# Performance work log

Hardware: AMD Instinct MI355X
Metric: run time of the kernel (lower is better)

The kernel has to match this reference:

```python
import jax, jax.numpy as jnp
import numpy as np

N_WIN = 8  # matches init kwarg n_win

def setup_inputs() -> dict:
    key = jax.random.key(0)
    k1, k2, k3 = jax.random.split(key, 3)
    c = 64
    x = jax.random.normal(k1, (1, c, 256, 256), dtype=jnp.float32)
    W = jax.random.normal(k2, (3 * c, c), dtype=jnp.float32) * 0.05
    bias = jax.random.normal(k3, (3 * c,), dtype=jnp.float32) * 0.05
    return {"x": x, "W": W, "bias": bias}

def reference(x, W, bias):
    b, c, h, w = x.shape
    n_h = n_w = N_WIN
    hs, ws = h // n_h, w // n_w
    nw = n_h * n_w
    # unfold into non-overlapping windows: [1, nw, hs*ws, c]
    xw = x.reshape(b, c, n_h, hs, n_w, ws)
    xw = xw.transpose(0, 2, 4, 3, 5, 1).reshape(1, nw, hs * ws, c)
    # shared QKV linear
    qkv = xw @ W.T + bias
    q, k, v = qkv[..., :c], qkv[..., c:2 * c], qkv[..., 2 * c:3 * c]
    # region-level routing via mean-pooled tokens
    q_r = q.mean(axis=2)  # [1, nw, c]
    k_r = k.mean(axis=2)
    a_r = jax.nn.relu(jnp.einsum('bic,bjc->bij', q_r, k_r))  # [1, nw, nw]
    # mix windows: a_r @ flattened(k/q) == window-mixing einsum
    k_m = jnp.einsum('bij,bjtc->bitc', a_r, k)
    q_m = jnp.einsum('bij,bjtc->bitc', a_r, q)
    # relu-gated windowed attention
    attn = jax.nn.relu(jnp.einsum('bitc,bisc->bits', q_m, k_m))  # [1, nw, T, T]
    o = jnp.einsum('bits,bisc->bitc', attn, v)  # [1, nw, T, c]
    # fold back to image
    o = o.reshape(b, n_h, n_w, hs, ws, c).transpose(0, 5, 1, 3, 2, 4).reshape(b, c, h, w)
    return o
```

## Files before the change

### kernel.cpp

```cpp
#include <hip/hip_runtime.h>

typedef _Float16 half_t;
typedef __attribute__((ext_vector_type(8))) _Float16 half8;
typedef __attribute__((ext_vector_type(4))) _Float16 half4;
typedef __attribute__((ext_vector_type(4))) float floatx4;
typedef __attribute__((ext_vector_type(16))) float floatx16;

#define MFMA16(A, B, C) __builtin_amdgcn_mfma_f32_16x16x32_f16((A), (B), (C), 0, 0, 0)
#define MFMA32(A, B, C) __builtin_amdgcn_mfma_f32_32x32x16_f16((A), (B), (C), 0, 0, 0)

__global__ __launch_bounds__(256) void k_qkv(
    const float* __restrict__ x, const float* __restrict__ W,
    const float* __restrict__ bias, half_t* __restrict__ q,
    half_t* __restrict__ k, half_t* __restrict__ vT,
    float* __restrict__ qsum, float* __restrict__ ksum) {
  __shared__ __align__(16) char smem[52736];
  half_t(*Xs)[72] = (half_t(*)[72])smem;
  half_t(*Ws)[72] = (half_t(*)[72])(smem + 18432);
  half_t(*S1)[136] = (half_t(*)[136])smem;
  half_t(*S2)[136] = (half_t(*)[136])(smem + 34816);
  float* qs_l = (float*)(smem + 52224);
  float* ks_l = qs_l + 64;
  const int w = blockIdx.y;
  const int tx = blockIdx.x;
  const int t0 = tx * 128;
  const int ih = w >> 3, iw = w & 7;
  const int xbase = ih * 8192 + iw * 32 + tx * 1024;
  const int tid = threadIdx.x;

  for (int i = tid; i < 2048; i += 256) {
    const int c = i >> 5, g = i & 31;
    const int tt = (g >> 3) * 32 + (g & 7) * 4;
    const floatx4 v =
        *(const floatx4*)&x[c * 65536 + xbase + (g >> 3) * 256 + (g & 7) * 4];
    #pragma unroll
    for (int p = 0; p < 4; p++) Xs[tt + p][c] = (half_t)v[p];
  }
  for (int i = tid; i < 3072; i += 256) {
    const int o = i >> 4, c4 = (i & 15) * 4;
    const floatx4 v = *(const floatx4*)&W[o * 64 + c4];
    half4 hv;
    #pragma unroll
    for (int p = 0; p < 4; p++) hv[p] = (half_t)v[p];
    *(half4*)&Ws[o][c4] = hv;
  }
  if (tid < 64) { qs_l[tid] = 0.f; ks_l[tid] = 0.f; }
  __syncthreads();

  const int wave = tid >> 6, lane = tid & 63;
  const int lrow = lane & 15, lq = lane >> 4;
  const int rbase = (wave >> 1) * 64;
  const int cbase = (wave & 1) * 96;

  floatx4 acc[4][6];
  const floatx4 z = {0.f, 0.f, 0.f, 0.f};
  #pragma unroll
  for (int mt = 0; mt < 4; mt++)
    #pragma unroll
    for (int nt = 0; nt < 6; nt++) acc[mt][nt] = z;

  #pragma unroll
  for (int kf = 0; kf < 2; kf++) {
    const int koff = kf * 32 + lq * 8;
    half8 a[4], b[6];
    #pragma unroll
    for (int mt = 0; mt < 4; mt++)
      a[mt] = *(const half8*)&Xs[rbase + mt * 16 + lrow][koff];
    #pragma unroll
    for (int nt = 0; nt < 6; nt++)
      b[nt] = *(const half8*)&Ws[cbase + nt * 16 + lrow][koff];
    #pragma unroll
    for (int mt = 0; mt < 4; mt++)
      #pragma unroll
      for (int nt = 0; nt < 6; nt++)
        acc[mt][nt] = MFMA16(a[mt], b[nt], acc[mt][nt]);
  }
  __syncthreads();

  #pragma unroll
  for (int nt = 0; nt < 6; nt++) {
    const int o = cbase + nt * 16 + lrow;
    const float bs = bias[o];
    if (o < 128) {
      float s = 0.f;
      #pragma unroll
      for (int mt = 0; mt < 4; mt++) {
        const int tr = rbase + mt * 16 + lq * 4;
        #pragma unroll
        for (int r = 0; r < 4; r++) {
          const float v = acc[mt][nt][r] + bs;
          S1[tr + r][o] = (half_t)v;
          s += v;
        }
      }
      if (o < 64) atomicAdd(&qs_l[o], s);
      else atomicAdd(&ks_l[o - 64], s);
    } else {
      const int oc = o - 128;
      #pragma unroll
      for (int mt = 0; mt < 4; mt++) {
        const int tr = rbase + mt * 16 + lq * 4;
        half4 pk;
        #pragma unroll
        for (int r = 0; r < 4; r++) pk[r] = (half_t)(acc[mt][nt][r] + bs);
        *(half4*)&S2[oc][tr] = pk;
      }
    }
  }
  __syncthreads();

  for (int idx = tid; idx < 3072; idx += 256) {
    if (idx < 2048) {
      const int t = idx >> 4, seg = idx & 15;
      const half8 v = *(const half8*)&S1[t][seg * 8];
      if (seg < 8)
        *(half8*)&q[w * 65536 + (t0 + t) * 64 + seg * 8] = v;
      else
        *(half8*)&k[w * 65536 + (t0 + t) * 64 + (seg - 8) * 8] = v;
    } else {
      const int i2 = idx - 2048;
      const int oc = i2 >> 4, seg = i2 & 15;
      *(half8*)&vT[w * 65536 + oc * 1024 + t0 + seg * 8] =
          *(const half8*)&S2[oc][seg * 8];
    }
  }
  if (tid < 64) {
    atomicAdd(&qsum[w * 64 + tid], qs_l[tid]);
    atomicAdd(&ksum[w * 64 + tid], ks_l[tid]);
  }
}

__global__ __launch_bounds__(256) void k_mix(const half_t* __restrict__ q,
                                             const half_t* __restrict__ k,
                                             const float* __restrict__ qsum,
                                             const float* __restrict__ ksum,
                                             half_t* __restrict__ qm,
                                             half_t* __restrict__ km) {
  __shared__ __align__(16) half_t qh[64][72];
  __shared__ __align__(16) half_t kh[64][72];
  __shared__ __align__(16) half_t arL[64][72];
  const half_t* __restrict__ src = blockIdx.y ? k : q;
  half_t* __restrict__ dst = blockIdx.y ? km : qm;
  const int tid = threadIdx.x;
  const int wave = tid >> 6, lane = tid & 63;
  const int ln31 = lane & 31;
  const int hk8 = (lane >> 5) * 8;
  const int lrow = lane & 15, lq = lane >> 4;

  const int pos0 = blockIdx.x * 256 + wave * 64 + ln31;
  half8 bB[2][4];
  #pragma unroll
  for (int t32 = 0; t32 < 2; t32++)
    #pragma unroll
    for (int kk = 0; kk < 4; kk++)
      #pragma unroll
      for (int jj = 0; jj < 8; jj++)
        bB[t32][kk][jj] =
            src[(kk * 16 + hk8 + jj) * 65536 + pos0 + t32 * 32];

  for (int e = tid; e < 1024; e += 256) {
    const int i = e >> 4, c4 = (e & 15) * 4;
    const floatx4 sq = *(const floatx4*)&qsum[i * 64 + c4];
    const floatx4 sk = *(const floatx4*)&ksum[i * 64 + c4];
    #pragma unroll
    for (int p = 0; p < 4; p++) {
      qh[i][c4 + p] = (half_t)sq[p];
      kh[i][c4 + p] = (half_t)sk[p];
    }
  }
  __syncthreads();

  {
    floatx4 ac[4];
    const floatx4 z = {0.f, 0.f, 0.f, 0.f};
    #pragma unroll
    for (int nt = 0; nt < 4; nt++) ac[nt] = z;
    #pragma unroll
    for (int kf = 0; kf < 2; kf++) {
      const int koff = kf * 32 + lq * 8;
      const half8 aF = *(const half8*)&qh[wave * 16 + lrow][koff];
      #pragma unroll
      for (int nt = 0; nt < 4; nt++) {
        const half8 bF = *(const half8*)&kh[nt * 16 + lrow][koff];
        ac[nt] = MFMA16(aF, bF, ac[nt]);
      }
    }
    const float scale = 1.f / (1024.f * 1024.f);
    #pragma unroll
    for (int nt = 0; nt < 4; nt++)
      #pragma unroll
      for (int r = 0; r < 4; r++) {
        const float v = ac[nt][r] * scale;
        arL[wave * 16 + lq * 4 + r][nt * 16 + lrow] =
            (half_t)(v > 0.f ? v : 0.f);
      }
  }
  __syncthreads();

  half8 aA[2][4];
  #pragma unroll
  for (int mt = 0; mt < 2; mt++)
    #pragma unroll
    for (int kk = 0; kk < 4; kk++)
      aA[mt][kk] = *(const half8*)&arL[mt * 32 + ln31][kk * 16 + hk8];

  #pragma unroll
  for (int t32 = 0; t32 < 2; t32++) {
    const int pos = pos0 + t32 * 32;
    floatx16 c0, c1;
    #pragma unroll
    for (int r = 0; r < 16; r++) { c0[r] = 0.f; c1[r] = 0.f; }
    #pragma unroll
    for (int kk = 0; kk < 4; kk++) {
      c0 = MFMA32(aA[0][kk], bB[t32][kk], c0);
      c1 = MFMA32(aA[1][kk], bB[t32][kk], c1);
    }
    const int h4 = (lane >> 5) * 4;
    #pragma unroll
    for (int r = 0; r < 16; r++) {
      const int row = (r & 3) + h4 + 8 * (r >> 2);
      dst[row * 65536 + pos] = (half_t)c0[r];
      dst[(32 + row) * 65536 + pos] = (half_t)c1[r];
    }
  }
}

__global__ __launch_bounds__(256, 2) void k_attn(const half_t* __restrict__ qm,
                                                 const half_t* __restrict__ km,
                                                 const half_t* __restrict__ vT,
                                                 float* __restrict__ out) {
  __shared__ __align__(16) char smem[55296];
  char* const VsB = smem;
  char* const StB = smem + 18432;
  const int w = blockIdx.x;
  const int t0 = blockIdx.y * 128;
  const int tid = threadIdx.x;
  const int wave = tid >> 6, lane = tid & 63;
  const int ln31 = lane & 31;
  const int hk8 = (lane >> 5) * 8, hk4 = (lane >> 5) * 4;
  const int w32 = wave * 32;
  const int wbase = w * 65536;

  auto vs_ptr = [&](int c, int sbyte) -> char* {
    return VsB + c * 288 + (sbyte ^ ((c & 15) << 4));
  };
  auto st_ptr = [&](int t, int sbyte) -> char* {
    return StB + t * 288 + (sbyte ^ ((t & 15) << 4));
  };

  half8 bQ[4][4];
  #pragma unroll
  for (int tt = 0; tt < 4; tt++)
    #pragma unroll
    for (int kk = 0; kk < 4; kk++)
      bQ[tt][kk] = *(const half8*)&qm[wbase + (t0 + tt * 32 + ln31) * 64 +
                                      kk * 16 + hk8];

  floatx16 oacc[2];
  #pragma unroll
  for (int ct = 0; ct < 2; ct++)
    #pragma unroll
    for (int r = 0; r < 16; r++) oacc[ct][r] = 0.f;

  half8 vpre[4], aK[4];
  #pragma unroll
  for (int j = 0; j < 4; j++) {
    const int idx = j * 256 + tid;
    const int c = idx >> 4, so = (idx & 15) * 8;
    vpre[j] = *(const half8*)&vT[wbase + c * 1024 + so];
  }
  #pragma unroll
  for (int kk = 0; kk < 4; kk++)
    aK[kk] = *(const half8*)&km[wbase + (w32 + ln31) * 64 + kk * 16 + hk8];

  for (int sc = 0; sc < 8; sc++) {
    floatx16 sacc[4];
    #pragma unroll
    for (int tt = 0; tt < 4; tt++)
      #pragma unroll
      for (int r = 0; r < 16; r++) sacc[tt][r] = 0.f;
    __builtin_amdgcn_s_setprio(1);
    #pragma unroll
    for (int kk = 0; kk < 4; kk++)
      #pragma unroll
      for (int tt = 0; tt < 4; tt++)
        sacc[tt] = MFMA32(aK[kk], bQ[tt][kk], sacc[tt]);
    __builtin_amdgcn_s_setprio(0);

    __syncthreads();

    #pragma unroll
    for (int j = 0; j < 4; j++) {
      const int idx = j * 256 + tid;
      const int c = idx >> 4;
      *(half8*)vs_ptr(c, (idx & 15) * 16) = vpre[j];
    }
    #pragma unroll
    for (int tt = 0; tt < 4; tt++) {
      const int t = tt * 32 + ln31;
      #pragma unroll
      for (int g = 0; g < 4; g++) {
        const int s = w32 + g * 8 + hk4;
        half4 pk;
        #pragma unroll
        for (int p = 0; p < 4; p++) {
          const float v = sacc[tt][g * 4 + p];
          pk[p] = (half_t)(v > 0.f ? v : 0.f);
        }
        *(half4*)st_ptr(t, s * 2) = pk;
      }
    }
    half8 aKn[4];
    if (sc < 7) {
      const int s0n = (sc + 1) * 128;
      #pragma unroll
      for (int j = 0; j < 4; j++) {
        const int idx = j * 256 + tid;
        const int c = idx >> 4, so = (idx & 15) * 8;
        vpre[j] = *(const half8*)&vT[wbase + c * 1024 + s0n + so];
      }
      #pragma unroll
      for (int kk = 0; kk < 4; kk++)
        aKn[kk] = *(const half8*)&km[wbase + (s0n + w32 + ln31) * 64 +
                                     kk * 16 + hk8];
    }
    __syncthreads();

    __builtin_amdgcn_s_setprio(1);
    #pragma unroll
    for (int kk = 0; kk < 8; kk++) {
      const half8 bS = *(const half8*)st_ptr(w32 + ln31, (kk * 16 + hk8) * 2);
      #pragma unroll
      for (int ct = 0; ct < 2; ct++) {
        const half8 aV =
            *(const half8*)vs_ptr(ct * 32 + ln31, (kk * 16 + hk8) * 2);
        oacc[ct] = MFMA32(aV, bS, oacc[ct]);
      }
    }
    __builtin_amdgcn_s_setprio(0);
    if (sc < 7) {
      #pragma unroll
      for (int kk = 0; kk < 4; kk++) aK[kk] = aKn[kk];
    }
  }

  const int ih = w >> 3, iw = w & 7;
  const int obase = ih * 8192 + iw * 32;
  const int tb = ((t0 + w32) >> 5) * 256 + ln31;
  const int h4 = (lane >> 5) * 4;
  #pragma unroll
  for (int ct = 0; ct < 2; ct++) {
    #pragma unroll
    for (int r = 0; r < 16; r++) {
      const int c = ct * 32 + (r & 3) + h4 + 8 * (r >> 2);
      out[c * 65536 + obase + tb] = oacc[ct][r];
    }
  }
}

extern "C" void kernel_launch(void* const* d_in, const int* in_sizes, int n_in,
                              void* d_out, int out_size, void* d_ws, size_t ws_size,
                              hipStream_t stream) {
  const float* x = (const float*)d_in[0];
  const float* W = (const float*)d_in[1];
  const float* bias = (const float*)d_in[2];
  float* out = (float*)d_out;

  half_t* q = (half_t*)d_ws;
  half_t* k = q + 4194304;
  half_t* vT = k + 4194304;
  half_t* qm = vT + 4194304;
  half_t* km = qm + 4194304;
  float* qsum = (float*)(km + 4194304);
  float* ksum = qsum + 4096;

  hipMemsetAsync(qsum, 0, 2 * 4096 * sizeof(float), stream);
  k_qkv<<<dim3(8, 64), 256, 0, stream>>>(x, W, bias, q, k, vT, qsum, ksum);
  k_mix<<<dim3(256, 2), 256, 0, stream>>>(q, k, qsum, ksum, qm, km);
  k_attn<<<dim3(64, 8), 256, 0, stream>>>(qm, km, vT, out);
}
```

Before: 116.4 us.

## Halve per-block tiles in qkv and mix kernels, use lgkm-only barrier in attn

The QKV projection kernel now processes 64 tokens per block instead of 128 and the window-mixing kernel 128 positions per block instead of 256, doubling their grid sizes to raise occupancy and parallelism across CUs. Shared memory in k_qkv shrinks accordingly. In the attention kernel, __syncthreads is replaced with a custom barrier that waits only on LDS counters (lgkmcnt) and not on outstanding global loads, so the V/K prefetches can stay in flight across the barrier. Smaller tiles add more redundant W loads and more atomics on the per-window sums.

```diff
diff --git a/kernel.cpp b/kernel.cpp
--- a/kernel.cpp
+++ b/kernel.cpp
@@ -9,30 +9,39 @@
 #define MFMA16(A, B, C) __builtin_amdgcn_mfma_f32_16x16x32_f16((A), (B), (C), 0, 0, 0)
 #define MFMA32(A, B, C) __builtin_amdgcn_mfma_f32_32x32x16_f16((A), (B), (C), 0, 0, 0)
 
+__device__ __forceinline__ void lds_barrier() {
+  __builtin_amdgcn_sched_barrier(0);
+  asm volatile("s_waitcnt lgkmcnt(0)\n\ts_barrier" ::: "memory");
+  __builtin_amdgcn_sched_barrier(0);
+}
+
 __global__ __launch_bounds__(256) void k_qkv(
     const float* __restrict__ x, const float* __restrict__ W,
     const float* __restrict__ bias, half_t* __restrict__ q,
     half_t* __restrict__ k, half_t* __restrict__ vT,
     float* __restrict__ qsum, float* __restrict__ ksum) {
-  __shared__ __align__(16) char smem[52736];
+  __shared__ __align__(16) char smem[37376];
   half_t(*Xs)[72] = (half_t(*)[72])smem;
-  half_t(*Ws)[72] = (half_t(*)[72])(smem + 18432);
+  half_t(*Ws)[72] = (half_t(*)[72])(smem + 9216);
   half_t(*S1)[136] = (half_t(*)[136])smem;
-  half_t(*S2)[136] = (half_t(*)[136])(smem + 34816);
-  float* qs_l = (float*)(smem + 52224);
+  half_t(*S2)[72] = (half_t(*)[72])(smem + 17408);
+  float* qs_l = (float*)(smem + 36864);
   float* ks_l = qs_l + 64;
   const int w = blockIdx.y;
   const int tx = blockIdx.x;
-  const int t0 = tx * 128;
+  const int t0 = tx * 64;
   const int ih = w >> 3, iw = w & 7;
-  const int xbase = ih * 8192 + iw * 32 + tx * 1024;
+  const int xoff = ih * 8192 + iw * 32;
   const int tid = threadIdx.x;
 
-  for (int i = tid; i < 2048; i += 256) {
-    const int c = i >> 5, g = i & 31;
-    const int tt = (g >> 3) * 32 + (g & 7) * 4;
+  #pragma unroll
+  for (int e = 0; e < 4; e++) {
+    const int i = e * 256 + tid;
+    const int c = i >> 4, g = i & 15;
+    const int h = g >> 3, f4 = g & 7;
     const floatx4 v =
-        *(const floatx4*)&x[c * 65536 + xbase + (g >> 3) * 256 + (g & 7) * 4];
+        *(const floatx4*)&x[c * 65536 + xoff + (tx * 2 + h) * 256 + f4 * 4];
+    const int tt = h * 32 + f4 * 4;
     #pragma unroll
     for (int p = 0; p < 4; p++) Xs[tt + p][c] = (half_t)v[p];
   }
@@ -49,28 +58,28 @@
 
   const int wave = tid >> 6, lane = tid & 63;
   const int lrow = lane & 15, lq = lane >> 4;
-  const int rbase = (wave >> 1) * 64;
+  const int rbase = (wave >> 1) * 32;
   const int cbase = (wave & 1) * 96;
 
-  floatx4 acc[4][6];
+  floatx4 acc[2][6];
   const floatx4 z = {0.f, 0.f, 0.f, 0.f};
   #pragma unroll
-  for (int mt = 0; mt < 4; mt++)
+  for (int mt = 0; mt < 2; mt++)
     #pragma unroll
     for (int nt = 0; nt < 6; nt++) acc[mt][nt] = z;
 
   #pragma unroll
   for (int kf = 0; kf < 2; kf++) {
     const int koff = kf * 32 + lq * 8;
-    half8 a[4], b[6];
-    #pragma unroll
-    for (int mt = 0; mt < 4; mt++)
+    half8 a[2], b[6];
+    #pragma unroll
+    for (int mt = 0; mt < 2; mt++)
       a[mt] = *(const half8*)&Xs[rbase + mt * 16 + lrow][koff];
     #pragma unroll
     for (int nt = 0; nt < 6; nt++)
       b[nt] = *(const half8*)&Ws[cbase + nt * 16 + lrow][koff];
     #pragma unroll
-    for (int mt = 0; mt < 4; mt++)
+    for (int mt = 0; mt < 2; mt++)
       #pragma unroll
       for (int nt = 0; nt < 6; nt++)
         acc[mt][nt] = MFMA16(a[mt], b[nt], acc[mt][nt]);
@@ -84,7 +93,7 @@
     if (o < 128) {
       float s = 0.f;
       #pragma unroll
-      for (int mt = 0; mt < 4; mt++) {
+      for (int mt = 0; mt < 2; mt++) {
         const int tr = rbase + mt * 16 + lq * 4;
         #pragma unroll
         for (int r = 0; r < 4; r++) {
@@ -98,7 +107,7 @@
     } else {
       const int oc = o - 128;
       #pragma unroll
-      for (int mt = 0; mt < 4; mt++) {
+      for (int mt = 0; mt < 2; mt++) {
         const int tr = rbase + mt * 16 + lq * 4;
         half4 pk;
         #pragma unroll
@@ -109,8 +118,8 @@
   }
   __syncthreads();
 
-  for (int idx = tid; idx < 3072; idx += 256) {
-    if (idx < 2048) {
+  for (int idx = tid; idx < 1536; idx += 256) {
+    if (idx < 1024) {
       const int t = idx >> 4, seg = idx & 15;
       const half8 v = *(const half8*)&S1[t][seg * 8];
       if (seg < 8)
@@ -118,8 +127,8 @@
       else
         *(half8*)&k[w * 65536 + (t0 + t) * 64 + (seg - 8) * 8] = v;
     } else {
-      const int i2 = idx - 2048;
-      const int oc = i2 >> 4, seg = i2 & 15;
+      const int i2 = idx - 1024;
+      const int oc = i2 >> 3, seg = i2 & 7;
       *(half8*)&vT[w * 65536 + oc * 1024 + t0 + seg * 8] =
           *(const half8*)&S2[oc][seg * 8];
     }
@@ -147,16 +156,13 @@
   const int hk8 = (lane >> 5) * 8;
   const int lrow = lane & 15, lq = lane >> 4;
 
-  const int pos0 = blockIdx.x * 256 + wave * 64 + ln31;
-  half8 bB[2][4];
-  #pragma unroll
-  for (int t32 = 0; t32 < 2; t32++)
-    #pragma unroll
-    for (int kk = 0; kk < 4; kk++)
-      #pragma unroll
-      for (int jj = 0; jj < 8; jj++)
-        bB[t32][kk][jj] =
-            src[(kk * 16 + hk8 + jj) * 65536 + pos0 + t32 * 32];
+  const int pos = blockIdx.x * 128 + wave * 32 + ln31;
+  half8 bB[4];
+  #pragma unroll
+  for (int kk = 0; kk < 4; kk++)
+    #pragma unroll
+    for (int jj = 0; jj < 8; jj++)
+      bB[kk][jj] = src[(kk * 16 + hk8 + jj) * 65536 + pos];
 
   for (int e = tid; e < 1024; e += 256) {
     const int i = e >> 4, c4 = (e & 15) * 4;
@@ -204,24 +210,20 @@
     for (int kk = 0; kk < 4; kk++)
       aA[mt][kk] = *(const half8*)&arL[mt * 32 + ln31][kk * 16 + hk8];
 
-  #pragma unroll
-  for (int t32 = 0; t32 < 2; t32++) {
-    const int pos = pos0 + t32 * 32;
-    floatx16 c0, c1;
-    #pragma unroll
-    for (int r = 0; r < 16; r++) { c0[r] = 0.f; c1[r] = 0.f; }
-    #pragma unroll
-    for (int kk = 0; kk < 4; kk++) {
-      c0 = MFMA32(aA[0][kk], bB[t32][kk], c0);
-      c1 = MFMA32(aA[1][kk], bB[t32][kk], c1);
-    }
-    const int h4 = (lane >> 5) * 4;
-    #pragma unroll
-    for (int r = 0; r < 16; r++) {
-      const int row = (r & 3) + h4 + 8 * (r >> 2);
-      dst[row * 65536 + pos] = (half_t)c0[r];
-      dst[(32 + row) * 65536 + pos] = (half_t)c1[r];
-    }
+  floatx16 c0, c1;
+  #pragma unroll
+  for (int r = 0; r < 16; r++) { c0[r] = 0.f; c1[r] = 0.f; }
+  #pragma unroll
+  for (int kk = 0; kk < 4; kk++) {
+    c0 = MFMA32(aA[0][kk], bB[kk], c0);
+    c1 = MFMA32(aA[1][kk], bB[kk], c1);
+  }
+  const int h4 = (lane >> 5) * 4;
+  #pragma unroll
+  for (int r = 0; r < 16; r++) {
+    const int row = (r & 3) + h4 + 8 * (r >> 2);
+    dst[row * 65536 + pos] = (half_t)c0[r];
+    dst[(32 + row) * 65536 + pos] = (half_t)c1[r];
   }
 }
 
@@ -287,7 +289,7 @@
         sacc[tt] = MFMA32(aK[kk], bQ[tt][kk], sacc[tt]);
     __builtin_amdgcn_s_setprio(0);
 
-    __syncthreads();
+    lds_barrier();
 
     #pragma unroll
     for (int j = 0; j < 4; j++) {
@@ -324,7 +326,7 @@
         aKn[kk] = *(const half8*)&km[wbase + (s0n + w32 + ln31) * 64 +
                                      kk * 16 + hk8];
     }
-    __syncthreads();
+    lds_barrier();
 
     __builtin_amdgcn_s_setprio(1);
     #pragma unroll
@@ -375,7 +377,7 @@
   float* ksum = qsum + 4096;
 
   hipMemsetAsync(qsum, 0, 2 * 4096 * sizeof(float), stream);
-  k_qkv<<<dim3(8, 64), 256, 0, stream>>>(x, W, bias, q, k, vT, qsum, ksum);
-  k_mix<<<dim3(256, 2), 256, 0, stream>>>(q, k, qsum, ksum, qm, km);
+  k_qkv<<<dim3(16, 64), 256, 0, stream>>>(x, W, bias, q, k, vT, qsum, ksum);
+  k_mix<<<dim3(512, 2), 256, 0, stream>>>(q, k, qsum, ksum, qm, km);
   k_attn<<<dim3(64, 8), 256, 0, stream>>>(qm, km, vT, out);
 }
```

Result: slower. 121.8 us (+4.7%).
